# Kernel tuning notes

Hardware: AMD Instinct MI355X
Metric: run time of the kernel (lower is better)

Reference implementation:

```python
import jax, jax.numpy as jnp
import numpy as np
from jax import lax

H = 64   # hidden_size
IN = 18  # input_size
L = 4    # lstm_layers
OUT = 3  # output_size
B = 2048
T = 512


def _lstm_layer(x, W_ih, W_hh, b_ih, b_hh):
    # x: [B,T,D]; PyTorch gate order: i, f, g, o
    xg = jnp.einsum('btd,gd->btg', x, W_ih) + b_ih + b_hh  # [B,T,4H]

    def step(carry, xg_t):
        h, c = carry
        gates = xg_t + h @ W_hh.T
        i, f, g, o = jnp.split(gates, 4, axis=-1)
        c = jax.nn.sigmoid(f) * c + jax.nn.sigmoid(i) * jnp.tanh(g)
        h = jax.nn.sigmoid(o) * jnp.tanh(c)
        return (h, c), h

    h0 = jnp.zeros((x.shape[0], H), x.dtype)
    _, hs = lax.scan(step, (h0, h0), jnp.swapaxes(xg, 0, 1))  # hs: [T,B,H]
    return jnp.swapaxes(hs, 0, 1)  # [B,T,H]


def _forward(x, Wi0, Wh0, bi0, bh0, Wi1, Wh1, bi1, bh1,
             Wi2, Wh2, bi2, bh2, Wi3, Wh3, bi3, bh3, W1, b1, W2, b2):
    h = x
    layers = [(Wi0, Wh0, bi0, bh0), (Wi1, Wh1, bi1, bh1),
              (Wi2, Wh2, bi2, bh2), (Wi3, Wh3, bi3, bh3)]
    for Wi, Wh, bi, bh in layers:
        h = _lstm_layer(h, Wi, Wh, bi, bh)
    last = h[:, -1, :]                      # [B,H]
    hid = jax.nn.relu(last @ W1.T + b1)     # [B,128]
    return hid @ W2.T + b2                  # [B,OUT]


def setup_inputs():
    key = jax.random.key(0)
    ks = jax.random.split(key, 1 + 4 * L + 4)
    d = {'x': jax.random.normal(ks[0], (B, T, IN), jnp.float32)}
    k = 1
    s = 0.1
    for l in range(L):
        din = IN if l == 0 else H
        d[f'Wi{l}'] = jax.random.normal(ks[k], (4 * H, din), jnp.float32) * s; k += 1
        d[f'Wh{l}'] = jax.random.normal(ks[k], (4 * H, H), jnp.float32) * s; k += 1
        d[f'bi{l}'] = jax.random.normal(ks[k], (4 * H,), jnp.float32) * s; k += 1
        d[f'bh{l}'] = jax.random.normal(ks[k], (4 * H,), jnp.float32) * s; k += 1
    d['W1'] = jax.random.normal(ks[k], (128, H), jnp.float32) * s; k += 1
    d['b1'] = jax.random.normal(ks[k], (128,), jnp.float32) * s; k += 1
    d['W2'] = jax.random.normal(ks[k], (OUT, 128), jnp.float32) * s; k += 1
    d['b2'] = jax.random.normal(ks[k], (OUT,), jnp.float32) * s
    return d


def reference(x, Wi0, Wh0, bi0, bh0, Wi1, Wh1, bi1, bh1,
              Wi2, Wh2, bi2, bh2, Wi3, Wh3, bi3, bh3, W1, b1, W2, b2):
    return _forward(x, Wi0, Wh0, bi0, bh0, Wi1, Wh1, bi1, bh1,
                    Wi2, Wh2, bi2, bh2, Wi3, Wh3, bi3, bh3, W1, b1, W2, b2)
```

## Files before the change

### kernel.cpp

```cpp
#include <hip/hip_runtime.h>
#include <stdint.h>

typedef __bf16 bf16_t;
typedef __bf16 bf16x8 __attribute__((ext_vector_type(8)));
typedef float  f32x4  __attribute__((ext_vector_type(4)));

union Frag { uint32_t u[4]; bf16x8 v; };

struct WPtrs {
    const float* Wi[4];
    const float* Wh[4];
    const float* bi[4];
    const float* bh[4];
};

#define LOG2E 1.44269504088896340736f

__device__ __forceinline__ float cell_c(float gi, float gf, float gg, float c) {
    const float ef = __builtin_amdgcn_exp2f(-gf);
    const float ei = __builtin_amdgcn_exp2f(-gi);
    const float Eg = __builtin_amdgcn_exp2f(gg);
    const float pf = 1.0f + ef, pi = 1.0f + ei;
    const float pg = Eg + 1.0f, mg = Eg - 1.0f;
    const float num = c * pi * pg + mg * pf;
    const float den = pf * pi * pg;
    return num * __builtin_amdgcn_rcpf(den);
}
__device__ __forceinline__ float cell_h(float go, float c) {
    const float Ec = __builtin_amdgcn_exp2f(c * (2.0f * LOG2E));
    const float eo = __builtin_amdgcn_exp2f(-go);
    const float num = Ec - 1.0f;
    const float den = (1.0f + eo) * (Ec + 1.0f);
    return num * __builtin_amdgcn_rcpf(den);
}

__device__ __forceinline__ float dpp_halfswap(float x) {
    int i = __float_as_int(x);
    int r = __builtin_amdgcn_update_dpp(i, i, 0x128 , 0xF, 0xF, false);
    return __int_as_float(r);
}

__device__ __forceinline__ void phase_barrier() {
    asm volatile("s_waitcnt lgkmcnt(0)" ::: "memory");
    __builtin_amdgcn_s_barrier();
    asm volatile("" ::: "memory");
}

__global__ __launch_bounds__(1024, 4)
void lstm_fused(const float* __restrict__ x0, float* __restrict__ last_out, WPtrs wp)
{
    const int tile = blockIdx.x;
    const int tid  = threadIdx.x;
    const int w    = tid >> 6;
    const int lane = tid & 63;
    const int l15  = lane & 15;
    const int l4   = lane >> 4;
    const int l    = w >> 2;
    const int uq   = w & 3;
    const bool hiH = (l15 >= 8);
    const int  col = l15 & 7;

    __shared__ uint2 lds_h[2][4][64][6];

    for (int i = tid; i < 2 * 4 * 64 * 6; i += 1024)
        ((uint2*)lds_h)[i] = make_uint2(0u, 0u);

    const float* Wi = wp.Wi[l];
    const float* Wh = wp.Wh[l];

    const float gs[4] = {LOG2E, LOG2E, 2.0f * LOG2E, LOG2E};

    bf16x8 whA[4][2];
    bf16x8 wiA[4][2];
#pragma unroll
    for (int G = 0; G < 4; ++G) {
        const float sc = gs[G];
        const int row = G * 64 + 16 * uq + l15;
        const float* r = Wh + (size_t)row * 64;
#pragma unroll
        for (int s = 0; s < 2; ++s) {
            f32x4 a = *(const f32x4*)(r + 32 * s + 4 * l4);
            f32x4 b = *(const f32x4*)(r + 32 * s + 4 * l4 + 16);
            bf16x8 f;
            f[0] = (bf16_t)(a[0] * sc); f[1] = (bf16_t)(a[1] * sc);
            f[2] = (bf16_t)(a[2] * sc); f[3] = (bf16_t)(a[3] * sc);
            f[4] = (bf16_t)(b[0] * sc); f[5] = (bf16_t)(b[1] * sc);
            f[6] = (bf16_t)(b[2] * sc); f[7] = (bf16_t)(b[3] * sc);
            whA[G][s] = f;
        }
        if (l == 0) {
            const float* ri = Wi + (size_t)row * 18;
            const int k0 = 4 * l4;
            bf16x8 f;
            f[0] = (bf16_t)(ri[k0 + 0] * sc); f[1] = (bf16_t)(ri[k0 + 1] * sc);
            f[2] = (bf16_t)(ri[k0 + 2] * sc); f[3] = (bf16_t)(ri[k0 + 3] * sc);
            f[4] = (l4 == 0) ? (bf16_t)(ri[16] * sc) : (bf16_t)0.0f;
            f[5] = (l4 == 0) ? (bf16_t)(ri[17] * sc) : (bf16_t)0.0f;
            f[6] = (bf16_t)0.0f; f[7] = (bf16_t)0.0f;
            wiA[G][0] = f;
            wiA[G][1] = f;
        } else {
            const float* ri = Wi + (size_t)row * 64;
#pragma unroll
            for (int s = 0; s < 2; ++s) {
                f32x4 a = *(const f32x4*)(ri + 32 * s + 4 * l4);
                f32x4 b = *(const f32x4*)(ri + 32 * s + 4 * l4 + 16);
                bf16x8 f;
                f[0] = (bf16_t)(a[0] * sc); f[1] = (bf16_t)(a[1] * sc);
                f[2] = (bf16_t)(a[2] * sc); f[3] = (bf16_t)(a[3] * sc);
                f[4] = (bf16_t)(b[0] * sc); f[5] = (bf16_t)(b[1] * sc);
                f[6] = (bf16_t)(b[2] * sc); f[7] = (bf16_t)(b[3] * sc);
                wiA[G][s] = f;
            }
        }
    }

    float biasA[4], biasB[4];
#pragma unroll
    for (int G = 0; G < 4; ++G) {
        const int rb = G * 64 + 16 * uq + 4 * l4 + (hiH ? 2 : 0);
        biasA[G] = (wp.bi[l][rb]     + wp.bh[l][rb])     * gs[G];
        biasB[G] = (wp.bi[l][rb + 1] + wp.bh[l][rb + 1]) * gs[G];
    }

    bf16x8& xfA = wiA[2][1];
    bf16x8& xfB = wiA[3][1];
    const int    xbatch = tile * 8 + (hiH ? 7 : col);
    const float* xrow   = x0 + (size_t)xbatch * (512 * 18);
    auto loadx = [&](int t, bf16x8& dst) {
        const float* xr = xrow + t * 18;
        const int k0 = 4 * l4;
        bf16x8 f;
        f[0] = (bf16_t)xr[k0 + 0]; f[1] = (bf16_t)xr[k0 + 1];
        f[2] = (bf16_t)xr[k0 + 2]; f[3] = (bf16_t)xr[k0 + 3];
        f[4] = (l4 == 0) ? (bf16_t)xr[16] : (bf16_t)0.0f;
        f[5] = (l4 == 0) ? (bf16_t)xr[17] : (bf16_t)0.0f;
        f[6] = (bf16_t)0.0f; f[7] = (bf16_t)0.0f;
        dst = f;
    };
    if (l == 0) { loadx(0, xfA); loadx(1, xfB); }

    float c0 = 0.0f, c1 = 0.0f;

    __syncthreads();

    auto phase = [&](int p, int br, int bw, bf16x8& xf) {
        const int t = p - l;
        if (t >= 0 && t < 512) {
            const f32x4 z4 = {0.0f, 0.0f, 0.0f, 0.0f};
            f32x4 acc[4];

            if (l == 0) {
#pragma unroll
                for (int G = 0; G < 4; ++G)
                    acc[G] = __builtin_amdgcn_mfma_f32_16x16x32_bf16(wiA[G][0], xf, z4, 0, 0, 0);
                loadx((t + 2) & 511, xf);
            } else {
                Frag b0, b1;
                {
                    uint4 q0 = *(const uint4*)&lds_h[br][l - 1][lane][0];
                    uint4 q1 = *(const uint4*)&lds_h[br][l - 1][lane][2];
                    b0.u[0] = q0.x; b0.u[1] = q0.y; b0.u[2] = q0.z; b0.u[3] = q0.w;
                    b1.u[0] = q1.x; b1.u[1] = q1.y; b1.u[2] = q1.z; b1.u[3] = q1.w;
                }
#pragma unroll
                for (int G = 0; G < 4; ++G)
                    acc[G] = __builtin_amdgcn_mfma_f32_16x16x32_bf16(wiA[G][0], b0.v, z4, 0, 0, 0);
#pragma unroll
                for (int G = 0; G < 4; ++G)
                    acc[G] = __builtin_amdgcn_mfma_f32_16x16x32_bf16(wiA[G][1], b1.v, acc[G], 0, 0, 0);
            }

            {
                Frag h0, h1;
                uint4 q0 = *(const uint4*)&lds_h[br][l][lane][0];
                uint4 q1 = *(const uint4*)&lds_h[br][l][lane][2];
                h0.u[0] = q0.x; h0.u[1] = q0.y; h0.u[2] = q0.z; h0.u[3] = q0.w;
                h1.u[0] = q1.x; h1.u[1] = q1.y; h1.u[2] = q1.z; h1.u[3] = q1.w;
#pragma unroll
                for (int G = 0; G < 4; ++G)
                    acc[G] = __builtin_amdgcn_mfma_f32_16x16x32_bf16(whA[G][0], h0.v, acc[G], 0, 0, 0);
#pragma unroll
                for (int G = 0; G < 4; ++G)
                    acc[G] = __builtin_amdgcn_mfma_f32_16x16x32_bf16(whA[G][1], h1.v, acc[G], 0, 0, 0);
            }

            float g0[4], g1[4];
#pragma unroll
            for (int G = 0; G < 4; ++G) {
                const float s2 = dpp_halfswap(acc[G][2]);
                const float s3 = dpp_halfswap(acc[G][3]);
                g0[G] = (hiH ? s2 : acc[G][0]) + biasA[G];
                g1[G] = (hiH ? s3 : acc[G][1]) + biasB[G];
            }

            const float cA = cell_c(g0[0], g0[1], g0[2], c0);
            const float cB = cell_c(g1[0], g1[1], g1[2], c1);
            c0 = cA; c1 = cB;
            const float hA = cell_h(g0[3], cA);
            const float hB = cell_h(g1[3], cB);

            union { uint32_t u; bf16_t b[2]; } pk;
            pk.b[0] = (bf16_t)hA; pk.b[1] = (bf16_t)hB;
            uint32_t* slot = (uint32_t*)&lds_h[bw][l][16 * l4 + col][uq];
            slot[hiH ? 1 : 0] = pk.u;

            if (l == 3 && t == 511) {
                float* o = last_out + ((size_t)(tile * 8 + col)) * 64
                           + 16 * uq + 4 * l4 + (hiH ? 2 : 0);
                *(float2*)o = make_float2(hA, hB);
            }
        }
        phase_barrier();
    };

    for (int p = 0; p < 516; p += 2) {
        phase(p,     1, 0, xfA);
        phase(p + 1, 0, 1, xfB);
    }
}

__global__ __launch_bounds__(256)
void mlp_head(const float* __restrict__ last,
              const float* __restrict__ W1, const float* __restrict__ b1,
              const float* __restrict__ W2, const float* __restrict__ b2,
              float* __restrict__ out)
{
    __shared__ float sW1[128 * 64];
    __shared__ float sb1[128];
    __shared__ float sW2[3 * 128];
    __shared__ float sb2[4];
    const int tid = threadIdx.x;
    for (int i = tid; i < 128 * 64; i += 256) sW1[i] = W1[i];
    for (int i = tid; i < 128; i += 256) sb1[i] = b1[i];
    for (int i = tid; i < 3 * 128; i += 256) sW2[i] = W2[i];
    if (tid < 3) sb2[tid] = b2[tid];
    __syncthreads();

    const int b = blockIdx.x * 256 + tid;
    const float* lb = last + (size_t)b * 64;
    float xv[64];
#pragma unroll
    for (int k = 0; k < 64; k += 4) {
        f32x4 v = *(const f32x4*)(lb + k);
        xv[k] = v[0]; xv[k + 1] = v[1]; xv[k + 2] = v[2]; xv[k + 3] = v[3];
    }
    float o0 = sb2[0], o1 = sb2[1], o2 = sb2[2];
    for (int j = 0; j < 128; ++j) {
        float a = sb1[j];
        const float* wr = &sW1[j * 64];
#pragma unroll
        for (int k = 0; k < 64; k += 4) {
            f32x4 wv = *(const f32x4*)(wr + k);
            a += xv[k] * wv[0] + xv[k + 1] * wv[1] + xv[k + 2] * wv[2] + xv[k + 3] * wv[3];
        }
        a = fmaxf(a, 0.0f);
        o0 += a * sW2[0 * 128 + j];
        o1 += a * sW2[1 * 128 + j];
        o2 += a * sW2[2 * 128 + j];
    }
    out[(size_t)b * 3 + 0] = o0;
    out[(size_t)b * 3 + 1] = o1;
    out[(size_t)b * 3 + 2] = o2;
}

extern "C" void kernel_launch(void* const* d_in, const int* in_sizes, int n_in,
                              void* d_out, int out_size, void* d_ws, size_t ws_size,
                              hipStream_t stream)
{
    (void)in_sizes; (void)n_in; (void)out_size; (void)ws_size;

    const float* x = (const float*)d_in[0];
    WPtrs wp;
    for (int l = 0; l < 4; ++l) {
        wp.Wi[l] = (const float*)d_in[1 + 4 * l + 0];
        wp.Wh[l] = (const float*)d_in[1 + 4 * l + 1];
        wp.bi[l] = (const float*)d_in[1 + 4 * l + 2];
        wp.bh[l] = (const float*)d_in[1 + 4 * l + 3];
    }
    const float* W1 = (const float*)d_in[17];
    const float* b1 = (const float*)d_in[18];
    const float* W2 = (const float*)d_in[19];
    const float* b2 = (const float*)d_in[20];

    float* last = (float*)d_ws;

    lstm_fused<<<dim3(256), dim3(1024), 0, stream>>>(x, last, wp);
    mlp_head<<<dim3(8), dim3(256), 0, stream>>>(last, W1, b1, W2, b2, (float*)d_out);
}
```

Baseline: 587.1 us.

## Stagger MFMA and cell-update halves across layers with two barriers per phase

```diff
diff --git a/kernel.cpp b/kernel.cpp
--- a/kernel.cpp
+++ b/kernel.cpp
@@ -61,13 +61,11 @@
     const int  col = l15 & 7;
 
     __shared__ uint2 lds_h[2][4][64][6];
-
     for (int i = tid; i < 2 * 4 * 64 * 6; i += 1024)
         ((uint2*)lds_h)[i] = make_uint2(0u, 0u);
 
     const float* Wi = wp.Wi[l];
     const float* Wh = wp.Wh[l];
-
     const float gs[4] = {LOG2E, LOG2E, 2.0f * LOG2E, LOG2E};
 
     bf16x8 whA[4][2];
@@ -125,8 +123,7 @@
 
     bf16x8& xfA = wiA[2][1];
     bf16x8& xfB = wiA[3][1];
-    const int    xbatch = tile * 8 + (hiH ? 7 : col);
-    const float* xrow   = x0 + (size_t)xbatch * (512 * 18);
+    const float* xrow = x0 + (size_t)(tile * 8 + (hiH ? 7 : col)) * (512 * 18);
     auto loadx = [&](int t, bf16x8& dst) {
         const float* xr = xrow + t * 18;
         const int k0 = 4 * l4;
@@ -142,79 +139,110 @@
 
     float c0 = 0.0f, c1 = 0.0f;
 
+    const int  sk    = (l == 0) ? 0 : (l == 1) ? 1 : (l == 2) ? 3 : 4;
+    const bool evenL = ((l & 1) == 0);
+
+    f32x4 acc[4];
+
     __syncthreads();
 
+    auto lds_frags = [&](int bi_, int ll_, Frag& f0, Frag& f1) {
+        uint4 q0 = *(const uint4*)&lds_h[bi_][ll_][lane][0];
+        uint4 q1 = *(const uint4*)&lds_h[bi_][ll_][lane][2];
+        f0.u[0] = q0.x; f0.u[1] = q0.y; f0.u[2] = q0.z; f0.u[3] = q0.w;
+        f1.u[0] = q1.x; f1.u[1] = q1.y; f1.u[2] = q1.z; f1.u[3] = q1.w;
+    };
+
+    auto mfma_even = [&](int br, bf16x8& xf, int tA) {
+        const f32x4 z4 = {0.0f, 0.0f, 0.0f, 0.0f};
+        __builtin_amdgcn_s_setprio(1);
+        if (l == 0) {
+#pragma unroll
+            for (int G = 0; G < 4; ++G)
+                acc[G] = __builtin_amdgcn_mfma_f32_16x16x32_bf16(wiA[G][0], xf, z4, 0, 0, 0);
+        } else {
+            Frag b0, b1; lds_frags(br, l - 1, b0, b1);
+#pragma unroll
+            for (int G = 0; G < 4; ++G)
+                acc[G] = __builtin_amdgcn_mfma_f32_16x16x32_bf16(wiA[G][0], b0.v, z4, 0, 0, 0);
+#pragma unroll
+            for (int G = 0; G < 4; ++G)
+                acc[G] = __builtin_amdgcn_mfma_f32_16x16x32_bf16(wiA[G][1], b1.v, acc[G], 0, 0, 0);
+        }
+        Frag h0, h1; lds_frags(br, l, h0, h1);
+#pragma unroll
+        for (int G = 0; G < 4; ++G)
+            acc[G] = __builtin_amdgcn_mfma_f32_16x16x32_bf16(whA[G][0], h0.v, acc[G], 0, 0, 0);
+#pragma unroll
+        for (int G = 0; G < 4; ++G)
+            acc[G] = __builtin_amdgcn_mfma_f32_16x16x32_bf16(whA[G][1], h1.v, acc[G], 0, 0, 0);
+        __builtin_amdgcn_s_setprio(0);
+        if (l == 0) loadx((tA + 2) & 511, xf);
+    };
+
+    auto mfma_odd = [&](int br, int bw) {
+        const f32x4 z4 = {0.0f, 0.0f, 0.0f, 0.0f};
+        __builtin_amdgcn_s_setprio(1);
+        Frag b0, b1; lds_frags(br, l - 1, b0, b1);
+#pragma unroll
+        for (int G = 0; G < 4; ++G)
+            acc[G] = __builtin_amdgcn_mfma_f32_16x16x32_bf16(wiA[G][0], b0.v, z4, 0, 0, 0);
+#pragma unroll
+        for (int G = 0; G < 4; ++G)
+            acc[G] = __builtin_amdgcn_mfma_f32_16x16x32_bf16(wiA[G][1], b1.v, acc[G], 0, 0, 0);
+        Frag h0, h1; lds_frags(bw, l, h0, h1);
+#pragma unroll
+        for (int G = 0; G < 4; ++G)
+            acc[G] = __builtin_amdgcn_mfma_f32_16x16x32_bf16(whA[G][0], h0.v, acc[G], 0, 0, 0);
+#pragma unroll
+        for (int G = 0; G < 4; ++G)
+            acc[G] = __builtin_amdgcn_mfma_f32_16x16x32_bf16(whA[G][1], h1.v, acc[G], 0, 0, 0);
+        __builtin_amdgcn_s_setprio(0);
+    };
+
+    auto do_cell = [&](int bw, int tt) {
+        float g0[4], g1[4];
+#pragma unroll
+        for (int G = 0; G < 4; ++G) {
+            const float s2 = dpp_halfswap(acc[G][2]);
+            const float s3 = dpp_halfswap(acc[G][3]);
+            g0[G] = (hiH ? s2 : acc[G][0]) + biasA[G];
+            g1[G] = (hiH ? s3 : acc[G][1]) + biasB[G];
+        }
+        const float cA = cell_c(g0[0], g0[1], g0[2], c0);
+        const float cB = cell_c(g1[0], g1[1], g1[2], c1);
+        c0 = cA; c1 = cB;
+        const float hA = cell_h(g0[3], cA);
+        const float hB = cell_h(g1[3], cB);
+        union { uint32_t u; bf16_t b[2]; } pk;
+        pk.b[0] = (bf16_t)hA; pk.b[1] = (bf16_t)hB;
+        uint32_t* slot = (uint32_t*)&lds_h[bw][l][16 * l4 + col][uq];
+        slot[hiH ? 1 : 0] = pk.u;
+        if (l == 3 && tt == 511) {
+            float* o = last_out + ((size_t)(tile * 8 + col)) * 64
+                       + 16 * uq + 4 * l4 + (hiH ? 2 : 0);
+            *(float2*)o = make_float2(hA, hB);
+        }
+    };
+
     auto phase = [&](int p, int br, int bw, bf16x8& xf) {
-        const int t = p - l;
-        if (t >= 0 && t < 512) {
-            const f32x4 z4 = {0.0f, 0.0f, 0.0f, 0.0f};
-            f32x4 acc[4];
-
-            if (l == 0) {
-#pragma unroll
-                for (int G = 0; G < 4; ++G)
-                    acc[G] = __builtin_amdgcn_mfma_f32_16x16x32_bf16(wiA[G][0], xf, z4, 0, 0, 0);
-                loadx((t + 2) & 511, xf);
-            } else {
-                Frag b0, b1;
-                {
-                    uint4 q0 = *(const uint4*)&lds_h[br][l - 1][lane][0];
-                    uint4 q1 = *(const uint4*)&lds_h[br][l - 1][lane][2];
-                    b0.u[0] = q0.x; b0.u[1] = q0.y; b0.u[2] = q0.z; b0.u[3] = q0.w;
-                    b1.u[0] = q1.x; b1.u[1] = q1.y; b1.u[2] = q1.z; b1.u[3] = q1.w;
-                }
-#pragma unroll
-                for (int G = 0; G < 4; ++G)
-                    acc[G] = __builtin_amdgcn_mfma_f32_16x16x32_bf16(wiA[G][0], b0.v, z4, 0, 0, 0);
-#pragma unroll
-                for (int G = 0; G < 4; ++G)
-                    acc[G] = __builtin_amdgcn_mfma_f32_16x16x32_bf16(wiA[G][1], b1.v, acc[G], 0, 0, 0);
-            }
-
-            {
-                Frag h0, h1;
-                uint4 q0 = *(const uint4*)&lds_h[br][l][lane][0];
-                uint4 q1 = *(const uint4*)&lds_h[br][l][lane][2];
-                h0.u[0] = q0.x; h0.u[1] = q0.y; h0.u[2] = q0.z; h0.u[3] = q0.w;
-                h1.u[0] = q1.x; h1.u[1] = q1.y; h1.u[2] = q1.z; h1.u[3] = q1.w;
-#pragma unroll
-                for (int G = 0; G < 4; ++G)
-                    acc[G] = __builtin_amdgcn_mfma_f32_16x16x32_bf16(whA[G][0], h0.v, acc[G], 0, 0, 0);
-#pragma unroll
-                for (int G = 0; G < 4; ++G)
-                    acc[G] = __builtin_amdgcn_mfma_f32_16x16x32_bf16(whA[G][1], h1.v, acc[G], 0, 0, 0);
-            }
-
-            float g0[4], g1[4];
-#pragma unroll
-            for (int G = 0; G < 4; ++G) {
-                const float s2 = dpp_halfswap(acc[G][2]);
-                const float s3 = dpp_halfswap(acc[G][3]);
-                g0[G] = (hiH ? s2 : acc[G][0]) + biasA[G];
-                g1[G] = (hiH ? s3 : acc[G][1]) + biasB[G];
-            }
-
-            const float cA = cell_c(g0[0], g0[1], g0[2], c0);
-            const float cB = cell_c(g1[0], g1[1], g1[2], c1);
-            c0 = cA; c1 = cB;
-            const float hA = cell_h(g0[3], cA);
-            const float hB = cell_h(g1[3], cB);
-
-            union { uint32_t u; bf16_t b[2]; } pk;
-            pk.b[0] = (bf16_t)hA; pk.b[1] = (bf16_t)hB;
-            uint32_t* slot = (uint32_t*)&lds_h[bw][l][16 * l4 + col][uq];
-            slot[hiH ? 1 : 0] = pk.u;
-
-            if (l == 3 && t == 511) {
-                float* o = last_out + ((size_t)(tile * 8 + col)) * 64
-                           + 16 * uq + 4 * l4 + (hiH ? 2 : 0);
-                *(float2*)o = make_float2(hA, hB);
-            }
+        const int tA = p - sk;
+        const int tC = p - 1 - sk;
+        if (evenL) {
+            if ((unsigned)tA < 512u) mfma_even(br, xf, tA);
+        } else {
+            if ((unsigned)tC < 512u) do_cell(bw, tC);
         }
         phase_barrier();
-    };
-
-    for (int p = 0; p < 516; p += 2) {
+        if (evenL) {
+            if ((unsigned)tA < 512u) do_cell(bw, tA);
+        } else {
+            if ((unsigned)tA < 512u) mfma_odd(br, bw);
+        }
+        phase_barrier();
+    };
+
+    for (int p = 0; p < 518; p += 2) {
         phase(p,     1, 0, xfA);
         phase(p + 1, 0, 1, xfB);
     }
```

After: 660.4 us. 1.12x slower.
